# Kernel optimization log

Measured on AMD Instinct MI355X. Metric: run time of the kernel, lower is better.

The kernel has to match this reference:

```python
import jax, jax.numpy as jnp
import numpy as np

B, L, D = 2, 2048, 1024
H = 16
DH = D // H
FACTOR = 0.6
U = max(1, min(L, int(FACTOR * L)))  # 1228 selected queries


def setup_inputs() -> dict:
    key = jax.random.key(0)
    ks = jax.random.split(key, 9)
    s = 0.02
    return {
        "x": jax.random.normal(ks[0], (B, L, D), dtype=jnp.float32),
        "Wq": jax.random.normal(ks[1], (D, D), dtype=jnp.float32) * s,
        "bq": jnp.zeros((D,), dtype=jnp.float32),
        "Wk": jax.random.normal(ks[2], (D, D), dtype=jnp.float32) * s,
        "bk": jnp.zeros((D,), dtype=jnp.float32),
        "Wv": jax.random.normal(ks[3], (D, D), dtype=jnp.float32) * s,
        "bv": jnp.zeros((D,), dtype=jnp.float32),
        "Wo": jax.random.normal(ks[4], (D, D), dtype=jnp.float32) * s,
        "bo": jnp.zeros((D,), dtype=jnp.float32),
    }


def _split_heads(x):
    b, l, d = x.shape
    return x.reshape(b, l, H, DH).transpose(0, 2, 1, 3)  # [b,h,l,dh]


def reference(x, Wq, bq, Wk, bk, Wv, bv, Wo, bo):
    b, l, _ = x.shape
    scale = 1.0 / jnp.sqrt(jnp.asarray(DH, dtype=x.dtype))

    q = _split_heads(x @ Wq + bq)  # [b,h,l,dh]
    k = _split_heads(x @ Wk + bk)
    v = _split_heads(x @ Wv + bv)

    # full scores for sparsity heuristic
    scores = jnp.einsum("bhqd,bhkd->bhqk", q, k) * scale  # [b,h,l,l]
    sparsity = scores.max(axis=-1) - scores.mean(axis=-1)  # [b,h,l]

    _, top_idx = jax.lax.top_k(sparsity, U)  # [b,h,U]

    # gather selected queries, attend only on those rows
    q_sel = jnp.take_along_axis(q, top_idx[..., None], axis=2)  # [b,h,U,dh]
    scores_sel = jnp.einsum("bhud,bhkd->bhuk", q_sel, k) * scale  # [b,h,U,l]
    attn = jax.nn.softmax(scores_sel, axis=-1)
    out_sel = jnp.einsum("bhuk,bhkd->bhud", attn, v)  # [b,h,U,dh]

    # scatter back into zero-initialized output
    bi = jnp.arange(b)[:, None, None]
    hi = jnp.arange(H)[None, :, None]
    out = jnp.zeros_like(q).at[bi, hi, top_idx].set(out_sel)  # [b,h,l,dh]

    out = out.transpose(0, 2, 1, 3).reshape(b, l, D)
    return out @ Wo + bo
```

## Files before the change

kernel.cpp:

```cpp
#include <hip/hip_runtime.h>
#include <math.h>
#include <stdint.h>

#define Bn 2
#define Ln 2048
#define Dn 1024
#define Hn 16
#define DHn 64
#define Un 1228
#define BHn (Bn*Hn)
#define SCALE 0.125f
#define SXf 16.0f
#define SWf 256.0f
#define SQf 16.0f
#define SVf 16.0f
#define SPf 16.0f
#define ESC_PROJ (1.0f / 4096.0f)
#define ESC_OUT  (1.0f / 65536.0f)
#define PSC (SCALE / 256.0f)
#define QPS 88

typedef _Float16 f16;
typedef __attribute__((ext_vector_type(8))) _Float16 f16x8;
typedef __attribute__((ext_vector_type(4))) float f32x4;
struct h4s { f16 x, y, z, w; };

__device__ __forceinline__ void splitf16(float f, f16& hi, f16& lo) {
  hi = (f16)f;
  lo = (f16)(f - (float)hi);
}

__device__ __forceinline__ void gl_lds16(const void* g, void* l) {
  __builtin_amdgcn_global_load_lds(
      (const __attribute__((address_space(1))) void*)g,
      (__attribute__((address_space(3))) void*)l, 16, 0, 0);
}

#define MFMA(a, b, c) __builtin_amdgcn_mfma_f32_16x16x32_f16((a), (b), (c), 0, 0, 0)

__global__ __launch_bounds__(256) void split_kernel(
    const float* __restrict__ in, f16* __restrict__ oh, f16* __restrict__ ol, int n4) {
  int i = blockIdx.x * 256 + threadIdx.x;
  if (i >= n4) return;
  float4 v = ((const float4*)in)[i];
  h4s h, l;
  splitf16(v.x * SXf, h.x, l.x); splitf16(v.y * SXf, h.y, l.y);
  splitf16(v.z * SXf, h.z, l.z); splitf16(v.w * SXf, h.w, l.w);
  ((h4s*)oh)[i] = h; ((h4s*)ol)[i] = l;
}

__global__ __launch_bounds__(256) void tsplit_w4(
    const float* __restrict__ W0, const float* __restrict__ W1,
    const float* __restrict__ W2, const float* __restrict__ W3,
    f16* __restrict__ oh, f16* __restrict__ ol) {
  __shared__ float ts[64][65];
  const int t = threadIdx.x;
  const int r0 = blockIdx.x * 64, c0 = blockIdx.y * 64;
  const int z = blockIdx.z;
  const float* in = (z == 0) ? W0 : (z == 1) ? W1 : (z == 2) ? W2 : W3;
#pragma unroll
  for (int c = 0; c < 4; ++c) {
    int f = (c * 256 + t) * 4; int row = f >> 6, col = f & 63;
    float4 v = *(const float4*)&in[(size_t)(r0 + row) * Dn + c0 + col];
    ts[row][col] = v.x; ts[row][col + 1] = v.y; ts[row][col + 2] = v.z; ts[row][col + 3] = v.w;
  }
  __syncthreads();
#pragma unroll
  for (int c = 0; c < 4; ++c) {
    int f = (c * 256 + t) * 4; int crow = f >> 6, rcol = f & 63;
    h4s h, l;
    splitf16(ts[rcol + 0][crow] * SWf, h.x, l.x);
    splitf16(ts[rcol + 1][crow] * SWf, h.y, l.y);
    splitf16(ts[rcol + 2][crow] * SWf, h.z, l.z);
    splitf16(ts[rcol + 3][crow] * SWf, h.w, l.w);
    size_t o = (size_t)(z * 1024 + c0 + crow) * Dn + r0 + rcol;
    *(h4s*)&oh[o] = h; *(h4s*)&ol[o] = l;
  }
}

__global__ void gemm_qkv(
    const f16* __restrict__ Ah, const f16* __restrict__ Al,
    const f16* __restrict__ Bth, const f16* __restrict__ Btl,
    const float* __restrict__ bq, const float* __restrict__ bk, const float* __restrict__ bv,
    float* __restrict__ Qf, f16* __restrict__ Qbh, f16* __restrict__ Qbl,
    float* __restrict__ Kf, f16* __restrict__ Kbh, f16* __restrict__ Kbl,
    f16* __restrict__ Vh16, int K) {
  __shared__ f16 sAh[128 * 32], sAl[128 * 32], sBh[128 * 32], sBl[128 * 32];
  const int t = threadIdx.x;
  const int w = t >> 6, lane = t & 63, lm = lane & 15, q = lane >> 4;
  const int wr = w >> 1, wc = w & 1;
  const int n0 = blockIdx.x * 128, m0 = blockIdx.y * 128;
  f32x4 acc[4][4] = {};
  for (int k0 = 0; k0 < K; k0 += 32) {
    const f16* s0 = Ah + (size_t)m0 * K + k0;
    const f16* s1 = Al + (size_t)m0 * K + k0;
    const f16* s2 = Bth + (size_t)n0 * K + k0;
    const f16* s3 = Btl + (size_t)n0 * K + k0;
#pragma unroll
    for (int c = 0; c < 2; ++c) {
      int f = (c * 256 + t) * 8; int row = f >> 5, col = f & 31;
      size_t go = (size_t)row * K + col;
      gl_lds16(s0 + go, &sAh[f]);
      gl_lds16(s1 + go, &sAl[f]);
      gl_lds16(s2 + go, &sBh[f]);
      gl_lds16(s3 + go, &sBl[f]);
    }
    __syncthreads();
    f16x8 a_h[4], a_l[4], b_h[4], b_l[4];
#pragma unroll
    for (int mi = 0; mi < 4; ++mi) {
      int r = (wr * 64 + mi * 16 + lm) * 32 + q * 8;
      a_h[mi] = *(const f16x8*)&sAh[r];
      a_l[mi] = *(const f16x8*)&sAl[r];
    }
#pragma unroll
    for (int ni = 0; ni < 4; ++ni) {
      int r = (wc * 64 + ni * 16 + lm) * 32 + q * 8;
      b_h[ni] = *(const f16x8*)&sBh[r];
      b_l[ni] = *(const f16x8*)&sBl[r];
    }
#pragma unroll
    for (int mi = 0; mi < 4; ++mi)
#pragma unroll
      for (int ni = 0; ni < 4; ++ni) {
        acc[mi][ni] = MFMA(a_h[mi], b_h[ni], acc[mi][ni]);
        acc[mi][ni] = MFMA(a_h[mi], b_l[ni], acc[mi][ni]);
        acc[mi][ni] = MFMA(a_l[mi], b_h[ni], acc[mi][ni]);
      }
    __syncthreads();
  }
#pragma unroll
  for (int mi = 0; mi < 4; ++mi)
#pragma unroll
    for (int ni = 0; ni < 4; ++ni) {
      int nglob = n0 + wc * 64 + ni * 16;
      int seg = nglob >> 10;
      int c = (nglob & 1023) + lm;
      const float* bp = (seg == 0) ? bq : (seg == 1) ? bk : bv;
      float bvv = bp[c];
#pragma unroll
      for (int r = 0; r < 4; ++r) {
        int grow = m0 + wr * 64 + mi * 16 + q * 4 + r;
        float v = acc[mi][ni][r] * ESC_PROJ + bvv;
        size_t o = (size_t)grow * 1024 + c;
        if (seg == 0) {
          Qf[o] = v;
          f16 hh, ll; splitf16(v * SQf, hh, ll); Qbh[o] = hh; Qbl[o] = ll;
        } else if (seg == 1) {
          Kf[o] = v;
          f16 hh, ll; splitf16(v * SQf, hh, ll); Kbh[o] = hh; Kbl[o] = ll;
        } else {
          Vh16[o] = (f16)(v * SVf);
        }
      }
    }
}

__global__ __launch_bounds__(256) void tsplit_v(
    const f16* __restrict__ Vh16, f16* __restrict__ out) {
  __shared__ f16 ts[64][72];
  const int t = threadIdx.x;
  const int l0 = blockIdx.x * 64;
  const int bh = blockIdx.y, b = bh >> 4, h = bh & 15;
#pragma unroll
  for (int c = 0; c < 2; ++c) {
    int e = c * 256 + t; int row = e >> 3, cg = e & 7;
    *(uint4*)&ts[row][cg * 8] =
        *(const uint4*)&Vh16[((size_t)b * Ln + l0 + row) * Dn + h * DHn + cg * 8];
  }
  __syncthreads();
#pragma unroll
  for (int c = 0; c < 2; ++c) {
    int e = c * 256 + t; int drow = e >> 3, lg = e & 7;
    f16 tmp[8];
#pragma unroll
    for (int j = 0; j < 8; ++j) tmp[j] = ts[lg * 8 + j][drow];
    *(uint4*)&out[((size_t)bh * DHn + drow) * Ln + l0 + lg * 8] = *(uint4*)tmp;
  }
}

__global__ __launch_bounds__(256, 4) void gemm_a1(
    const f16* __restrict__ A,
    const f16* __restrict__ Bth, const f16* __restrict__ Btl,
    const float* __restrict__ bias, float escale,
    float* __restrict__ Cf, int M, int N, int K) {
  __shared__ f16 sA[128 * 32], sBh[64 * 32], sBl[64 * 32];
  const int t = threadIdx.x;
  const int w = t >> 6, lane = t & 63, lm = lane & 15, q = lane >> 4;
  const int wr = w >> 1, wc = w & 1;
  const int n0 = blockIdx.x * 64, m0 = blockIdx.y * 128;
  f32x4 acc[4][2] = {};
  for (int k0 = 0; k0 < K; k0 += 32) {
    const f16* s0 = A + (size_t)m0 * K + k0;
    const f16* s2 = Bth + (size_t)n0 * K + k0;
    const f16* s3 = Btl + (size_t)n0 * K + k0;
#pragma unroll
    for (int c = 0; c < 2; ++c) {
      int f = (c * 256 + t) * 8; int row = f >> 5, col = f & 31;
      gl_lds16(s0 + (size_t)row * K + col, &sA[f]);
    }
    {
      int f = t * 8; int row = f >> 5, col = f & 31;
      gl_lds16(s2 + (size_t)row * K + col, &sBh[f]);
      gl_lds16(s3 + (size_t)row * K + col, &sBl[f]);
    }
    __syncthreads();
    f16x8 a_[4], b_h[2], b_l[2];
#pragma unroll
    for (int mi = 0; mi < 4; ++mi)
      a_[mi] = *(const f16x8*)&sA[(wr * 64 + mi * 16 + lm) * 32 + q * 8];
#pragma unroll
    for (int ni = 0; ni < 2; ++ni) {
      int r = (wc * 32 + ni * 16 + lm) * 32 + q * 8;
      b_h[ni] = *(const f16x8*)&sBh[r];
      b_l[ni] = *(const f16x8*)&sBl[r];
    }
#pragma unroll
    for (int mi = 0; mi < 4; ++mi)
#pragma unroll
      for (int ni = 0; ni < 2; ++ni) {
        acc[mi][ni] = MFMA(a_[mi], b_h[ni], acc[mi][ni]);
        acc[mi][ni] = MFMA(a_[mi], b_l[ni], acc[mi][ni]);
      }
    __syncthreads();
  }
#pragma unroll
  for (int mi = 0; mi < 4; ++mi)
#pragma unroll
    for (int ni = 0; ni < 2; ++ni) {
      int gcol = n0 + wc * 32 + ni * 16 + lm;
      float bvv = bias[gcol];
#pragma unroll
      for (int r = 0; r < 4; ++r) {
        int grow = m0 + wr * 64 + mi * 16 + q * 4 + r;
        Cf[(size_t)grow * N + gcol] = acc[mi][ni][r] * escale + bvv;
      }
    }
}

__global__ __launch_bounds__(256) void ksum_part(
    const f16* __restrict__ Kh, const f16* __restrict__ Kl, float* __restrict__ ksum) {
  __shared__ float red[4][64];
  const int t = threadIdx.x, d = t & 63, seg = t >> 6;
  const int bx = blockIdx.x, bh = blockIdx.y, b = bh >> 4, h = bh & 15;
  float s = 0.f;
  const int lbase = bx * 256 + seg * 64;
  for (int r = 0; r < 64; ++r) {
    size_t o = ((size_t)b * Ln + lbase + r) * Dn + h * DHn + d;
    s += (float)Kh[o] + (float)Kl[o];
  }
  red[seg][d] = s;
  __syncthreads();
  if (t < 64) atomicAdd(&ksum[bh * DHn + t], red[0][t] + red[1][t] + red[2][t] + red[3][t]);
}

__global__ __launch_bounds__(256, 2) void attn_stats_mfma(
    const f16* __restrict__ Qh, const f16* __restrict__ Ql,
    const f16* __restrict__ Kh, const f16* __restrict__ Kl,
    const float* __restrict__ ksum,
    float* __restrict__ row_max, float* __restrict__ spars) {
  __shared__ f16 sQh[128 * 64], sQl[128 * 64], sKh[128 * 64], sKl[128 * 64];
  __shared__ float redm[128][5];
  const int t = threadIdx.x;
  const int w = t >> 6, lane = t & 63, lm = lane & 15, q = lane >> 4;
  const int bh = blockIdx.y, b = bh >> 4, h = bh & 15;
  const int q0 = blockIdx.x * 128;
  const f16* qsh = Qh + ((size_t)b * Ln + q0) * Dn + h * DHn;
  const f16* qsl = Ql + ((size_t)b * Ln + q0) * Dn + h * DHn;
#pragma unroll
  for (int c = 0; c < 4; ++c) {
    int f = (c * 256 + t) * 8; int row = f >> 6, c16 = (f >> 3) & 7;
    size_t go = (size_t)row * Dn + ((c16 ^ (row & 7)) << 3);
    gl_lds16(qsh + go, &sQh[f]);
    gl_lds16(qsl + go, &sQl[f]);
  }
  __syncthreads();
  f16x8 a_h[8][2], a_l[8][2];
#pragma unroll
  for (int mi = 0; mi < 8; ++mi)
#pragma unroll
    for (int ks = 0; ks < 2; ++ks) {
      int row = mi * 16 + lm;
      int r = row * 64 + (((ks * 4 + q) ^ (row & 7)) << 3);
      a_h[mi][ks] = *(const f16x8*)&sQh[r];
      a_l[mi][ks] = *(const f16x8*)&sQl[r];
    }
  float rmax[8][4];
#pragma unroll
  for (int mi = 0; mi < 8; ++mi)
#pragma unroll
    for (int r = 0; r < 4; ++r) rmax[mi][r] = -1e30f;

  for (int kt = 0; kt < Ln / 128; ++kt) {
    __syncthreads();
    const f16* ksh = Kh + ((size_t)b * Ln + kt * 128) * Dn + h * DHn;
    const f16* ksl = Kl + ((size_t)b * Ln + kt * 128) * Dn + h * DHn;
#pragma unroll
    for (int c = 0; c < 4; ++c) {
      int f = (c * 256 + t) * 8; int row = f >> 6, c16 = (f >> 3) & 7;
      size_t go = (size_t)row * Dn + ((c16 ^ (row & 7)) << 3);
      gl_lds16(ksh + go, &sKh[f]);
      gl_lds16(ksl + go, &sKl[f]);
    }
    __syncthreads();
#pragma unroll
    for (int ni = 0; ni < 2; ++ni) {
      int bcol = (w * 2 + ni) * 16;
      f16x8 b_h[2], b_l[2];
#pragma unroll
      for (int ks = 0; ks < 2; ++ks) {
        int row = bcol + lm;
        int r = row * 64 + (((ks * 4 + q) ^ (row & 7)) << 3);
        b_h[ks] = *(const f16x8*)&sKh[r];
        b_l[ks] = *(const f16x8*)&sKl[r];
      }
#pragma unroll
      for (int mi = 0; mi < 8; ++mi) {
        f32x4 acc = {0.f, 0.f, 0.f, 0.f};
        __builtin_amdgcn_s_setprio(1);
#pragma unroll
        for (int ks = 0; ks < 2; ++ks) {
          acc = MFMA(a_h[mi][ks], b_h[ks], acc);
          acc = MFMA(a_h[mi][ks], b_l[ks], acc);
          acc = MFMA(a_l[mi][ks], b_h[ks], acc);
        }
        __builtin_amdgcn_s_setprio(0);
#pragma unroll
        for (int r = 0; r < 4; ++r) rmax[mi][r] = fmaxf(rmax[mi][r], acc[r]);
      }
    }
  }
#pragma unroll
  for (int mi = 0; mi < 8; ++mi)
#pragma unroll
    for (int r = 0; r < 4; ++r) {
      float v = rmax[mi][r];
      v = fmaxf(v, __shfl_xor(v, 1)); v = fmaxf(v, __shfl_xor(v, 2));
      v = fmaxf(v, __shfl_xor(v, 4)); v = fmaxf(v, __shfl_xor(v, 8));
      if (lm == 0) redm[mi * 16 + q * 4 + r][w] = v;
    }
  __syncthreads();
  if (t < 128) {
    float m = fmaxf(fmaxf(redm[t][0], redm[t][1]), fmaxf(redm[t][2], redm[t][3]));
    float dot = 0.f;
    const float* kp = ksum + bh * DHn;
#pragma unroll
    for (int d = 0; d < 64; ++d) {
      int idx = t * 64 + ((((d >> 3) ^ (t & 7)) << 3) | (d & 7));
      dot += ((float)sQh[idx] + (float)sQl[idx]) * kp[d];
    }
    row_max[(size_t)bh * Ln + q0 + t] = m * PSC;
    spars[(size_t)bh * Ln + q0 + t] = m * PSC - dot * (PSC / (float)Ln);
  }
}

__global__ __launch_bounds__(1024) void topk_sort(
    const float* __restrict__ spars, int* __restrict__ top_idx, int* __restrict__ wrow) {
  __shared__ unsigned long long keys[Ln];
  const int t = threadIdx.x;
  const int bh = blockIdx.x;
  for (int i = t; i < Ln; i += 1024) {
    unsigned u = __float_as_uint(spars[(size_t)bh * Ln + i]);
    u = (u & 0x80000000u) ? ~u : (u | 0x80000000u);
    u = ~u;
    keys[i] = ((unsigned long long)u << 32) | (unsigned)i;
  }
  __syncthreads();
  for (int k = 2; k <= Ln; k <<= 1) {
    for (int j = k >> 1; j > 0; j >>= 1) {
      int i = ((t & ~(j - 1)) << 1) | (t & (j - 1));
      int ixj = i | j;
      unsigned long long a = keys[i], bb = keys[ixj];
      bool up = ((i & k) == 0);
      if ((a > bb) == up) { keys[i] = bb; keys[ixj] = a; }
      __syncthreads();
    }
  }
  for (int u = t; u < Un - 8; u += 1024)
    top_idx[(size_t)bh * Un + u] = (int)(keys[u] & 0xFFFFFFFFu);
  if (t < 16) wrow[bh * 16 + t] = (int)(keys[Un - 8 + t] & 0xFFFFFFFFu);
}

__global__ __launch_bounds__(256) void refine_rows(
    const float* __restrict__ Qf, const float* __restrict__ Kf,
    const int* __restrict__ wrow, float* __restrict__ spx) {
  __shared__ float qs[64];
  __shared__ float redm[4], reds[4];
  const int t = threadIdx.x;
  const int j = blockIdx.x, bh = blockIdx.y, b = bh >> 4, h = bh & 15;
  const int qi = wrow[bh * 16 + j];
  if (t < 64) qs[t] = Qf[((size_t)b * Ln + qi) * Dn + h * DHn + t];
  __syncthreads();
  float mx = -1e30f, sm = 0.f;
  for (int ki = t; ki < Ln; ki += 256) {
    const float* kp = &Kf[((size_t)b * Ln + ki) * Dn + h * DHn];
    float s = 0.f;
#pragma unroll
    for (int d0 = 0; d0 < 64; d0 += 4) {
      float4 k4 = *(const float4*)&kp[d0];
      s = fmaf(k4.x, qs[d0], s);
      s = fmaf(k4.y, qs[d0 + 1], s);
      s = fmaf(k4.z, qs[d0 + 2], s);
      s = fmaf(k4.w, qs[d0 + 3], s);
    }
    mx = fmaxf(mx, s); sm += s;
  }
  const int w = t >> 6, lane = t & 63;
#pragma unroll
  for (int off = 1; off < 64; off <<= 1) {
    mx = fmaxf(mx, __shfl_xor(mx, off));
    sm += __shfl_xor(sm, off);
  }
  if (lane == 0) { redm[w] = mx; reds[w] = sm; }
  __syncthreads();
  if (t == 0) {
    float m = fmaxf(fmaxf(redm[0], redm[1]), fmaxf(redm[2], redm[3]));
    float s = reds[0] + reds[1] + reds[2] + reds[3];
    spx[bh * 16 + j] = SCALE * (m - s * (1.0f / (float)Ln));
  }
}

__global__ __launch_bounds__(64) void topk_final(
    const float* __restrict__ spx, const int* __restrict__ wrow,
    int* __restrict__ top_idx) {
  const int bh = blockIdx.x;
  if (threadIdx.x != 0) return;
  float v[16]; int r[16];
#pragma unroll
  for (int j = 0; j < 16; ++j) { v[j] = spx[bh * 16 + j]; r[j] = wrow[bh * 16 + j]; }
  unsigned taken = 0;
  for (int s = 0; s < 8; ++s) {
    int best = -1;
    for (int j = 0; j < 16; ++j) {
      if (taken & (1u << j)) continue;
      if (best < 0 || v[j] > v[best] || (v[j] == v[best] && r[j] < r[best])) best = j;
    }
    taken |= 1u << best;
    top_idx[(size_t)bh * Un + (Un - 8) + s] = r[best];
  }
}

__global__ __launch_bounds__(256, 4) void attn_sel_part(
    const f16* __restrict__ Qh, const f16* __restrict__ Kh,
    const f16* __restrict__ Vth,
    const int* __restrict__ topi, const float* __restrict__ row_max,
    float* __restrict__ pO, float* __restrict__ pD) {
  __shared__ f16 sK[64 * 64], sV[64 * 64];
  __shared__ f16 sQP[64 * QPS];
  __shared__ float rmL[64];
  __shared__ int qxL[64];
  __shared__ float dred[64][5];
  const int t = threadIdx.x;
  const int w = t >> 6, lane = t & 63, lm = lane & 15, q = lane >> 4;
  const int half = blockIdx.y & 1, bh = blockIdx.y >> 1, b = bh >> 4, h = bh & 15;
  const int u0 = blockIdx.x * 64;
  const int nrows = (Un - u0 < 64) ? (Un - u0) : 64;
  if (t < 64) {
    int qi = topi[(size_t)bh * Un + ((t < nrows) ? (u0 + t) : 0)];
    qxL[t] = qi;
    rmL[t] = row_max[(size_t)bh * Ln + qi];
  }
  __syncthreads();
#pragma unroll
  for (int c = 0; c < 2; ++c) {
    int f = (c * 256 + t) * 8; int row = f >> 6, col = f & 63;
    size_t go = ((size_t)b * Ln + qxL[row]) * Dn + h * DHn + col;
    *(uint4*)&sQP[row * QPS + col] = *(const uint4*)&Qh[go];
  }
  __syncthreads();
  f16x8 aq[4][2];
#pragma unroll
  for (int mi = 0; mi < 4; ++mi)
#pragma unroll
    for (int ks = 0; ks < 2; ++ks)
      aq[mi][ks] = *(const f16x8*)&sQP[(mi * 16 + lm) * QPS + ks * 32 + q * 8];
  f32x4 oacc[4] = {};
  float dacc[4][4] = {};

  const f16* kbase = Kh + (size_t)b * Ln * Dn + h * DHn;
  const f16* vbase = Vth + (size_t)bh * DHn * Ln;
  for (int kt = 0; kt < 16; ++kt) {
    const int l0 = half * 1024 + kt * 64;
    __syncthreads();
#pragma unroll
    for (int c = 0; c < 2; ++c) {
      int f = (c * 256 + t) * 8; int row = f >> 6, c16 = (f >> 3) & 7;
      int sc = (c16 ^ (row & 7)) << 3;
      gl_lds16(kbase + (size_t)(l0 + row) * Dn + sc, &sK[f]);
      gl_lds16(vbase + (size_t)row * Ln + l0 + sc, &sV[f]);
    }
    __syncthreads();
    f16x8 kb[2];
#pragma unroll
    for (int ks = 0; ks < 2; ++ks) {
      int row = w * 16 + lm;
      kb[ks] = *(const f16x8*)&sK[row * 64 + (((ks * 4 + q) ^ (row & 7)) << 3)];
    }
#pragma unroll
    for (int mi = 0; mi < 4; ++mi) {
      f32x4 acc = {0.f, 0.f, 0.f, 0.f};
      __builtin_amdgcn_s_setprio(1);
      acc = MFMA(aq[mi][0], kb[0], acc);
      acc = MFMA(aq[mi][1], kb[1], acc);
      __builtin_amdgcn_s_setprio(0);
#pragma unroll
      for (int r = 0; r < 4; ++r) {
        int row = mi * 16 + q * 4 + r;
        float p = __expf(acc[r] * PSC - rmL[row]);
        dacc[mi][r] += p;
        sQP[row * QPS + w * 16 + lm] = (f16)(p * SPf);
      }
    }
    __syncthreads();
    f16x8 vb[2];
#pragma unroll
    for (int ks = 0; ks < 2; ++ks) {
      int row = w * 16 + lm;
      vb[ks] = *(const f16x8*)&sV[row * 64 + (((ks * 4 + q) ^ (row & 7)) << 3)];
    }
#pragma unroll
    for (int mi = 0; mi < 4; ++mi) {
      f16x8 pf0 = *(const f16x8*)&sQP[(mi * 16 + lm) * QPS + 0 * 32 + q * 8];
      f16x8 pf1 = *(const f16x8*)&sQP[(mi * 16 + lm) * QPS + 1 * 32 + q * 8];
      __builtin_amdgcn_s_setprio(1);
      oacc[mi] = MFMA(pf0, vb[0], oacc[mi]);
      oacc[mi] = MFMA(pf1, vb[1], oacc[mi]);
      __builtin_amdgcn_s_setprio(0);
    }
  }
#pragma unroll
  for (int mi = 0; mi < 4; ++mi)
#pragma unroll
    for (int r = 0; r < 4; ++r) {
      float v = dacc[mi][r];
      v += __shfl_xor(v, 1); v += __shfl_xor(v, 2);
      v += __shfl_xor(v, 4); v += __shfl_xor(v, 8);
      if (lm == 0) dred[mi * 16 + q * 4 + r][w] = v;
    }
  __syncthreads();
  const size_t pbase = ((size_t)half * BHn + bh) * 1280 + u0;
  if (t < 64)
    pD[pbase + t] = dred[t][0] + dred[t][1] + dred[t][2] + dred[t][3];
#pragma unroll
  for (int mi = 0; mi < 4; ++mi)
#pragma unroll
    for (int r = 0; r < 4; ++r) {
      int row = mi * 16 + q * 4 + r;
      pO[(pbase + row) * 64 + w * 16 + lm] = oacc[mi][r];
    }
}

__global__ __launch_bounds__(256) void attn_combine(
    const float* __restrict__ pO, const float* __restrict__ pD,
    const int* __restrict__ topi, f16* __restrict__ AOh) {
  const int t = threadIdx.x;
  const int u0 = blockIdx.x * 64, bh = blockIdx.y, b = bh >> 4, h = bh & 15;
  const int nrows = (Un - u0 < 64) ? (Un - u0) : 64;
  const int row = t >> 2, pg = t & 3;
  if (row >= nrows) return;
  int qi = topi[(size_t)bh * Un + u0 + row];
  size_t i0 = (size_t)bh * 1280 + u0 + row;
  size_t i1 = (size_t)BHn * 1280 + i0;
  float dinv = 1.0f / (pD[i0] + pD[i1]);
  const float* p0 = &pO[i0 * 64 + pg * 16];
  const float* p1 = &pO[i1 * 64 + pg * 16];
  f16 buf[16];
#pragma unroll
  for (int c = 0; c < 4; ++c) {
    float4 a = *(const float4*)&p0[c * 4];
    float4 bb = *(const float4*)&p1[c * 4];
    buf[c * 4 + 0] = (f16)((a.x + bb.x) * dinv);
    buf[c * 4 + 1] = (f16)((a.y + bb.y) * dinv);
    buf[c * 4 + 2] = (f16)((a.z + bb.z) * dinv);
    buf[c * 4 + 3] = (f16)((a.w + bb.w) * dinv);
  }
  f16* dst = &AOh[((size_t)b * Ln + qi) * Dn + h * DHn + pg * 16];
  *(uint4*)&dst[0] = *(uint4*)&buf[0];
  *(uint4*)&dst[8] = *(uint4*)&buf[8];
}

extern "C" void kernel_launch(void* const* d_in, const int* in_sizes, int n_in,
                              void* d_out, int out_size, void* d_ws, size_t ws_size,
                              hipStream_t stream) {
  (void)in_sizes; (void)n_in; (void)out_size; (void)ws_size;
  const float* x  = (const float*)d_in[0];
  const float* Wq = (const float*)d_in[1];
  const float* bq = (const float*)d_in[2];
  const float* Wk = (const float*)d_in[3];
  const float* bk = (const float*)d_in[4];
  const float* Wv = (const float*)d_in[5];
  const float* bv = (const float*)d_in[6];
  const float* Wo = (const float*)d_in[7];
  const float* bo = (const float*)d_in[8];
  float* out = (float*)d_out;

  uint8_t* p = (uint8_t*)d_ws;
  const size_t NE = (size_t)Bn * Ln * Dn;
  f16* xh = (f16*)p;  p += NE * 2;
  f16* xl = (f16*)p;  p += NE * 2;
  f16* Wt_h = (f16*)p; p += (size_t)4096 * Dn * 2;
  f16* Wt_l = (f16*)p; p += (size_t)4096 * Dn * 2;
  f16* Qbh = (f16*)p; p += NE * 2;
  f16* Qbl = (f16*)p; p += NE * 2;
  f16* Kbh = (f16*)p; p += NE * 2;
  f16* Kbl = (f16*)p; p += NE * 2;
  float* Qf = (float*)p;  p += NE * 4;
  float* Kf = (float*)p;  p += NE * 4;
  f16* Vh16 = (f16*)p; p += NE * 2;
  f16* Vth  = (f16*)p; p += NE * 2;
  float* rowmax = (float*)p; p += (size_t)BHn * Ln * 4;
  float* spars  = (float*)p; p += (size_t)BHn * Ln * 4;
  float* ksum   = (float*)p; p += (size_t)BHn * DHn * 4;
  int* topi     = (int*)p;   p += (size_t)BHn * Un * 4;
  int* wrow     = (int*)p;   p += (size_t)BHn * 16 * 4;
  float* spx    = (float*)p; p += (size_t)BHn * 16 * 4;
  float* pD     = (float*)p; p += (size_t)2 * BHn * 1280 * 4;
  float* pO = Qf;
  f16* AOh = xh;

  dim3 blk(256);
  hipLaunchKernelGGL(split_kernel, dim3((int)(NE / 4 / 256)), blk, 0, stream, x, xh, xl, (int)(NE / 4));
  hipLaunchKernelGGL(tsplit_w4, dim3(16, 16, 4), blk, 0, stream, Wq, Wk, Wv, Wo, Wt_h, Wt_l);
  hipLaunchKernelGGL(gemm_qkv, dim3(24, 32), blk, 0, stream, xh, xl, Wt_h, Wt_l,
                     bq, bk, bv, Qf, Qbh, Qbl, Kf, Kbh, Kbl, Vh16, Dn);
  hipLaunchKernelGGL(tsplit_v, dim3(Ln / 64, BHn), blk, 0, stream, Vh16, Vth);
  hipMemsetAsync(ksum, 0, (size_t)BHn * DHn * 4, stream);
  hipLaunchKernelGGL(ksum_part, dim3(8, BHn), blk, 0, stream, Kbh, Kbl, ksum);
  hipLaunchKernelGGL(attn_stats_mfma, dim3(Ln / 128, BHn), blk, 0, stream,
                     Qbh, Qbl, Kbh, Kbl, ksum, rowmax, spars);
  hipLaunchKernelGGL(topk_sort, dim3(BHn), dim3(1024), 0, stream, spars, topi, wrow);
  hipLaunchKernelGGL(refine_rows, dim3(16, BHn), blk, 0, stream, Qf, Kf, wrow, spx);
  hipLaunchKernelGGL(topk_final, dim3(BHn), dim3(64), 0, stream, spx, wrow, topi);
  hipMemsetAsync(AOh, 0, NE * 2, stream);
  hipLaunchKernelGGL(attn_sel_part, dim3((Un + 63) / 64, 2 * BHn), blk, 0, stream,
                     Qbh, Kbh, Vth, topi, rowmax, pO, pD);
  hipLaunchKernelGGL(attn_combine, dim3((Un + 63) / 64, BHn), blk, 0, stream,
                     pO, pD, topi, AOh);
  hipLaunchKernelGGL(gemm_a1, dim3(16, 32), blk, 0, stream, AOh,
                     Wt_h + (size_t)3072 * Dn, Wt_l + (size_t)3072 * Dn, bo,
                     ESC_OUT, out, Bn * Ln, Dn, Dn);
}
```

Before: 393.9 us.

## Rewrite QKV projection GEMM with double-buffered LDS pipeline and XCD-aware block remap

Replaces the simple single-buffered split-f16 QKV GEMM with a software-pipelined kernel. It uses a 64-wide K step, double-buffered LDS with XOR swizzle, and async global-to-LDS loads issued in phases interleaved with MFMA. It also uses explicit barriers and waitcnts, setprio around the MFMA bursts, and a block index remap across XCDs. The three split terms are flattened into a 48-stage sequence over K. The goal is to hide global memory latency and LDS bank conflicts in the projection GEMM, at the cost of hand-scheduled code that is harder to maintain and fragile if the dimensions change.

```diff
diff --git a/kernel.cpp b/kernel.cpp
--- a/kernel.cpp
+++ b/kernel.cpp
@@ -78,57 +78,110 @@
   }
 }
 
-__global__ void gemm_qkv(
+#define QKV_STAGE(T, u) do { \
+    const int term_ = (T) >> 4; \
+    const int chunk_ = (u) >> 1, half_ = (u) & 1; \
+    const f16* s_; \
+    if (chunk_ < 2) s_ = ((term_ == 1) ? Btl : Bth) + (size_t)(n0 + chunk_ * 64) * Dn; \
+    else            s_ = ((term_ == 2) ? Al : Ah) + (size_t)(m0 + (chunk_ - 2) * 64) * Dn; \
+    s_ += (size_t)((T) & 15) * 64 + (size_t)(half_ * 32) * Dn + goff; \
+    gl_lds16(s_, &lds[((((T) & 1) << 2) + chunk_) * 4096 + half_ * 2048 + ldst]); \
+  } while (0)
+
+#define QKV_RDA(BB, MH) do { \
+    _Pragma("unroll") for (int m2_ = 0; m2_ < 2; ++m2_) { \
+      int lr_ = ((MH) * 2 + m2_) * 16 + lm; \
+      const f16* p_ = &lds[(BB) + (2 + wr) * 4096 + lr_ * 64]; \
+      a_[m2_][0] = *(const f16x8*)(p_ + kx0); \
+      a_[m2_][1] = *(const f16x8*)(p_ + kx1); \
+    } } while (0)
+
+#define QKV_RDB(BB, NH) do { \
+    _Pragma("unroll") for (int n2_ = 0; n2_ < 2; ++n2_) { \
+      int lr_ = ((NH) * 2 + n2_) * 16 + lm; \
+      const f16* p_ = &lds[(BB) + wc * 4096 + lr_ * 64]; \
+      b_[NH][n2_][0] = *(const f16x8*)(p_ + kx0); \
+      b_[NH][n2_][1] = *(const f16x8*)(p_ + kx1); \
+    } } while (0)
+
+#define QKV_MM(MH, NH) do { \
+    _Pragma("unroll") for (int m2_ = 0; m2_ < 2; ++m2_) \
+    _Pragma("unroll") for (int n2_ = 0; n2_ < 2; ++n2_) { \
+      f32x4& A_ = acc[(MH) * 2 + m2_][(NH) * 2 + n2_]; \
+      A_ = MFMA(a_[m2_][0], b_[(NH)][n2_][0], A_); \
+      A_ = MFMA(a_[m2_][1], b_[(NH)][n2_][1], A_); \
+    } } while (0)
+
+#define QKV_PHASE(BB, MH, NH, ISS, TG, U0, VM) do { \
+    if ((MH) == 0 && (NH) == 0) { QKV_RDA(BB, 0); QKV_RDB(BB, 0); } \
+    else if ((MH) == 0 && (NH) == 1) { QKV_RDB(BB, 1); } \
+    else if ((MH) == 1 && (NH) == 0) { QKV_RDA(BB, 1); } \
+    if (ISS) { QKV_STAGE(TG, U0); QKV_STAGE(TG, (U0) + 1); } \
+    asm volatile("" ::: "memory"); \
+    __builtin_amdgcn_s_barrier(); \
+    asm volatile("s_waitcnt lgkmcnt(0)" ::: "memory"); \
+    __builtin_amdgcn_sched_barrier(0); \
+    __builtin_amdgcn_s_setprio(1); \
+    QKV_MM(MH, NH); \
+    __builtin_amdgcn_s_setprio(0); \
+    if ((VM) == 1) asm volatile("s_waitcnt vmcnt(4)" ::: "memory"); \
+    if ((VM) == 2) asm volatile("s_waitcnt vmcnt(0)" ::: "memory"); \
+    asm volatile("" ::: "memory"); \
+    __builtin_amdgcn_s_barrier(); \
+  } while (0)
+
+__global__ __launch_bounds__(256, 2) void gemm_qkv8(
     const f16* __restrict__ Ah, const f16* __restrict__ Al,
     const f16* __restrict__ Bth, const f16* __restrict__ Btl,
     const float* __restrict__ bq, const float* __restrict__ bk, const float* __restrict__ bv,
     float* __restrict__ Qf, f16* __restrict__ Qbh, f16* __restrict__ Qbl,
     float* __restrict__ Kf, f16* __restrict__ Kbh, f16* __restrict__ Kbl,
-    f16* __restrict__ Vh16, int K) {
-  __shared__ f16 sAh[128 * 32], sAl[128 * 32], sBh[128 * 32], sBl[128 * 32];
+    f16* __restrict__ Vh16) {
+  __shared__ f16 lds[32768];
   const int t = threadIdx.x;
   const int w = t >> 6, lane = t & 63, lm = lane & 15, q = lane >> 4;
   const int wr = w >> 1, wc = w & 1;
-  const int n0 = blockIdx.x * 128, m0 = blockIdx.y * 128;
+  int ob = blockIdx.x;
+  int wg = (ob & 7) * 96 + (ob >> 3);
+  const int bx = wg % 24, by = wg / 24;
+  const int n0 = bx * 128, m0 = by * 128;
+  const int srow = t >> 3;
+  const size_t goff = (size_t)srow * Dn + (size_t)((((t & 7) ^ (srow & 7)) << 3));
+  const int ldst = t * 8;
+  const int kx0 = ((q ^ (lm & 7)) << 3);
+  const int kx1 = (((4 + q) ^ (lm & 7)) << 3);
+
   f32x4 acc[4][4] = {};
-  for (int k0 = 0; k0 < K; k0 += 32) {
-    const f16* s0 = Ah + (size_t)m0 * K + k0;
-    const f16* s1 = Al + (size_t)m0 * K + k0;
-    const f16* s2 = Bth + (size_t)n0 * K + k0;
-    const f16* s3 = Btl + (size_t)n0 * K + k0;
-#pragma unroll
-    for (int c = 0; c < 2; ++c) {
-      int f = (c * 256 + t) * 8; int row = f >> 5, col = f & 31;
-      size_t go = (size_t)row * K + col;
-      gl_lds16(s0 + go, &sAh[f]);
-      gl_lds16(s1 + go, &sAl[f]);
-      gl_lds16(s2 + go, &sBh[f]);
-      gl_lds16(s3 + go, &sBl[f]);
-    }
-    __syncthreads();
-    f16x8 a_h[4], a_l[4], b_h[4], b_l[4];
-#pragma unroll
-    for (int mi = 0; mi < 4; ++mi) {
-      int r = (wr * 64 + mi * 16 + lm) * 32 + q * 8;
-      a_h[mi] = *(const f16x8*)&sAh[r];
-      a_l[mi] = *(const f16x8*)&sAl[r];
-    }
-#pragma unroll
-    for (int ni = 0; ni < 4; ++ni) {
-      int r = (wc * 64 + ni * 16 + lm) * 32 + q * 8;
-      b_h[ni] = *(const f16x8*)&sBh[r];
-      b_l[ni] = *(const f16x8*)&sBl[r];
-    }
-#pragma unroll
-    for (int mi = 0; mi < 4; ++mi)
-#pragma unroll
-      for (int ni = 0; ni < 4; ++ni) {
-        acc[mi][ni] = MFMA(a_h[mi], b_h[ni], acc[mi][ni]);
-        acc[mi][ni] = MFMA(a_h[mi], b_l[ni], acc[mi][ni]);
-        acc[mi][ni] = MFMA(a_l[mi], b_h[ni], acc[mi][ni]);
-      }
-    __syncthreads();
-  }
+  f16x8 a_[2][2], b_[2][2][2];
+
+  QKV_STAGE(0, 0); QKV_STAGE(0, 1); QKV_STAGE(0, 2); QKV_STAGE(0, 3);
+  QKV_STAGE(0, 4); QKV_STAGE(0, 5); QKV_STAGE(0, 6); QKV_STAGE(0, 7);
+  QKV_STAGE(1, 0); QKV_STAGE(1, 1); QKV_STAGE(1, 2); QKV_STAGE(1, 3);
+  asm volatile("s_waitcnt vmcnt(4)" ::: "memory");
+  asm volatile("" ::: "memory");
+  __builtin_amdgcn_s_barrier();
+
+#pragma unroll 1
+  for (int i = 0; i < 23; ++i) {
+    const int T1 = 2 * i + 1, T2 = 2 * i + 2, T3 = 2 * i + 3;
+    QKV_PHASE(0,     0, 0, 1, T1, 4, 0);
+    QKV_PHASE(0,     0, 1, 1, T1, 6, 0);
+    QKV_PHASE(0,     1, 0, 1, T2, 0, 0);
+    QKV_PHASE(0,     1, 1, 1, T2, 2, 1);
+    QKV_PHASE(16384, 0, 0, 1, T2, 4, 0);
+    QKV_PHASE(16384, 0, 1, 1, T2, 6, 0);
+    QKV_PHASE(16384, 1, 0, 1, T3, 0, 0);
+    QKV_PHASE(16384, 1, 1, 1, T3, 2, 1);
+  }
+  QKV_PHASE(0,     0, 0, 1, 47, 4, 0);
+  QKV_PHASE(0,     0, 1, 1, 47, 6, 0);
+  QKV_PHASE(0,     1, 0, 0, 0, 0, 0);
+  QKV_PHASE(0,     1, 1, 0, 0, 0, 2);
+  QKV_PHASE(16384, 0, 0, 0, 0, 0, 0);
+  QKV_PHASE(16384, 0, 1, 0, 0, 0, 0);
+  QKV_PHASE(16384, 1, 0, 0, 0, 0, 0);
+  QKV_PHASE(16384, 1, 1, 0, 0, 0, 0);
+
 #pragma unroll
   for (int mi = 0; mi < 4; ++mi)
 #pragma unroll
@@ -142,15 +195,15 @@
       for (int r = 0; r < 4; ++r) {
         int grow = m0 + wr * 64 + mi * 16 + q * 4 + r;
         float v = acc[mi][ni][r] * ESC_PROJ + bvv;
-        size_t o = (size_t)grow * 1024 + c;
+        size_t o2 = (size_t)grow * 1024 + c;
         if (seg == 0) {
-          Qf[o] = v;
-          f16 hh, ll; splitf16(v * SQf, hh, ll); Qbh[o] = hh; Qbl[o] = ll;
+          Qf[o2] = v;
+          f16 hh, ll; splitf16(v * SQf, hh, ll); Qbh[o2] = hh; Qbl[o2] = ll;
         } else if (seg == 1) {
-          Kf[o] = v;
-          f16 hh, ll; splitf16(v * SQf, hh, ll); Kbh[o] = hh; Kbl[o] = ll;
+          Kf[o2] = v;
+          f16 hh, ll; splitf16(v * SQf, hh, ll); Kbh[o2] = hh; Kbl[o2] = ll;
         } else {
-          Vh16[o] = (f16)(v * SVf);
+          Vh16[o2] = (f16)(v * SVf);
         }
       }
     }
@@ -621,8 +674,8 @@
   dim3 blk(256);
   hipLaunchKernelGGL(split_kernel, dim3((int)(NE / 4 / 256)), blk, 0, stream, x, xh, xl, (int)(NE / 4));
   hipLaunchKernelGGL(tsplit_w4, dim3(16, 16, 4), blk, 0, stream, Wq, Wk, Wv, Wo, Wt_h, Wt_l);
-  hipLaunchKernelGGL(gemm_qkv, dim3(24, 32), blk, 0, stream, xh, xl, Wt_h, Wt_l,
-                     bq, bk, bv, Qf, Qbh, Qbl, Kf, Kbh, Kbl, Vh16, Dn);
+  hipLaunchKernelGGL(gemm_qkv8, dim3(768), dim3(256), 0, stream, xh, xl, Wt_h, Wt_l,
+                     bq, bk, bv, Qf, Qbh, Qbl, Kf, Kbh, Kbl, Vh16);
   hipLaunchKernelGGL(tsplit_v, dim3(Ln / 64, BHn), blk, 0, stream, Vh16, Vth);
   hipMemsetAsync(ksum, 0, (size_t)BHn * DHn * 4, stream);
   hipLaunchKernelGGL(ksum_part, dim3(8, BHn), blk, 0, stream, Kbh, Kbl, ksum);
```

Measured after the change: 409.1 us. 3.8% more time.

## Add 8-wave pipelined QKV GEMM with double-buffered LDS and interleaved MFMA phases

Applied to the files above, without the earlier changes.

Adds a new QKV projection GEMM kernel using 512 threads (8 waves) per 128x128 tile. It stages hi/lo split operands into 128KB of double-buffered dynamic LDS with XOR swizzling and direct global-to-LDS loads. Each k-tile is split into six barrier-separated phases that interleave LDS reads, prefetch of the next tiles and MFMA work, with setprio, and uses an XCD-aware block remap. The goal is to hide global memory latency and raise MFMA utilisation in the largest GEMM. It falls back to the old kernel if the large shared-memory attribute cannot be set, and the hand-tuned waitcnt/barrier schedule carries a correctness risk.

```diff
diff --git a/kernel.cpp b/kernel.cpp
--- a/kernel.cpp
+++ b/kernel.cpp
@@ -151,6 +151,147 @@
           f16 hh, ll; splitf16(v * SQf, hh, ll); Kbh[o] = hh; Kbl[o] = ll;
         } else {
           Vh16[o] = (f16)(v * SVf);
+        }
+      }
+    }
+}
+
+#define Q8_STAGE(T, u) do { \
+    const f16* s_; \
+    if ((u) < 2)      s_ = Bth + (size_t)(n0 + (u) * 64) * Dn; \
+    else if ((u) < 4) s_ = Btl + (size_t)(n0 + ((u) - 2) * 64) * Dn; \
+    else if ((u) < 6) s_ = Ah + (size_t)(m0 + ((u) - 4) * 64) * Dn; \
+    else              s_ = Al + (size_t)(m0 + ((u) - 6) * 64) * Dn; \
+    s_ += (size_t)(T) * 64 + goff; \
+    gl_lds16(s_, &lds[(((T) & 1) << 15) + (u) * 4096 + ldst]); \
+  } while (0)
+
+#define Q8_RDA(BB, ARRC, MH, DST) do { \
+    _Pragma("unroll") for (int m2_ = 0; m2_ < 2; ++m2_) { \
+      int lr_ = (MH) * 32 + m2_ * 16 + lm; \
+      const f16* p_ = &lds[(BB) + ((ARRC) + wr) * 4096 + lr_ * 64]; \
+      DST[m2_][0] = *(const f16x8*)(p_ + kx0); \
+      DST[m2_][1] = *(const f16x8*)(p_ + kx1); \
+    } } while (0)
+
+#define Q8_RDB(BB, CH, DST) do { \
+    _Pragma("unroll") for (int n2_ = 0; n2_ < 2; ++n2_) { \
+      int row_ = wc * 32 + n2_ * 16 + lm; \
+      const f16* p_ = &lds[(BB) + ((CH) + (row_ >> 6)) * 4096 + (row_ & 63) * 64]; \
+      DST[n2_][0] = *(const f16x8*)(p_ + kx0); \
+      DST[n2_][1] = *(const f16x8*)(p_ + kx1); \
+    } } while (0)
+
+#define Q8_MM(ASET, BSET, MH) do { \
+    _Pragma("unroll") for (int m2_ = 0; m2_ < 2; ++m2_) \
+    _Pragma("unroll") for (int n2_ = 0; n2_ < 2; ++n2_) { \
+      f32x4& A_ = acc[(MH) * 2 + m2_][n2_]; \
+      A_ = MFMA(ASET[m2_][0], BSET[n2_][0], A_); \
+      A_ = MFMA(ASET[m2_][1], BSET[n2_][1], A_); \
+    } } while (0)
+
+#define Q8_MID do { \
+    asm volatile("" ::: "memory"); \
+    __builtin_amdgcn_s_barrier(); \
+    asm volatile("s_waitcnt lgkmcnt(0)" ::: "memory"); \
+    __builtin_amdgcn_sched_barrier(0); \
+    __builtin_amdgcn_s_setprio(1); \
+  } while (0)
+
+#define Q8_END(VM) do { \
+    __builtin_amdgcn_s_setprio(0); \
+    if ((VM) == 1) asm volatile("s_waitcnt vmcnt(4)" ::: "memory"); \
+    if ((VM) == 2) asm volatile("s_waitcnt vmcnt(0)" ::: "memory"); \
+    asm volatile("" ::: "memory"); \
+    __builtin_amdgcn_s_barrier(); \
+  } while (0)
+
+#define Q8_TILE(T, S1, S2, VME) do { \
+    const int BB_ = ((T) & 1) << 15; \
+     \
+    Q8_RDA(BB_, 4, 0, aA); Q8_RDB(BB_, 0, b_h); \
+    if (S1) Q8_STAGE((T) + 1, 4); \
+    Q8_MID; Q8_MM(aA, b_h, 0); Q8_END(0); \
+     \
+    Q8_RDA(BB_, 4, 1, aB); \
+    if (S1) Q8_STAGE((T) + 1, 5); \
+    Q8_MID; Q8_MM(aB, b_h, 1); Q8_END(0); \
+     \
+    Q8_RDB(BB_, 2, b_l); \
+    if (S1) { Q8_STAGE((T) + 1, 6); Q8_STAGE((T) + 1, 7); } \
+    Q8_MID; Q8_MM(aB, b_l, 1); Q8_END(0); \
+     \
+    if (S2) Q8_STAGE((T) + 2, 0); \
+    Q8_MID; Q8_MM(aA, b_l, 0); Q8_END(0); \
+     \
+    Q8_RDA(BB_, 6, 0, aA); \
+    if (S2) Q8_STAGE((T) + 2, 1); \
+    Q8_MID; Q8_MM(aA, b_h, 0); Q8_END(0); \
+     \
+    Q8_RDA(BB_, 6, 1, aB); \
+    if (S2) { Q8_STAGE((T) + 2, 2); Q8_STAGE((T) + 2, 3); } \
+    Q8_MID; Q8_MM(aB, b_h, 1); Q8_END(VME); \
+  } while (0)
+
+__global__ __launch_bounds__(512, 2) void gemm_qkv8(
+    const f16* __restrict__ Ah, const f16* __restrict__ Al,
+    const f16* __restrict__ Bth, const f16* __restrict__ Btl,
+    const float* __restrict__ bq, const float* __restrict__ bk, const float* __restrict__ bv,
+    float* __restrict__ Qf, f16* __restrict__ Qbh, f16* __restrict__ Qbl,
+    float* __restrict__ Kf, f16* __restrict__ Kbh, f16* __restrict__ Kbl,
+    f16* __restrict__ Vh16) {
+  extern __shared__ f16 lds[];
+  const int t = threadIdx.x;
+  const int w = t >> 6, lane = t & 63, lm = lane & 15, q = lane >> 4;
+  const int wr = w >> 2, wc = w & 3;
+  int ob = blockIdx.x;
+  int wg = (ob & 7) * 96 + (ob >> 3);
+  const int bx = wg % 24, by = wg / 24;
+  const int n0 = bx * 128, m0 = by * 128;
+  const int srow = t >> 3;
+  const size_t goff = (size_t)srow * Dn + (size_t)((((t & 7) ^ (srow & 7)) << 3));
+  const int ldst = t * 8;
+  const int kx0 = ((q ^ (lm & 7)) << 3);
+  const int kx1 = (((4 + q) ^ (lm & 7)) << 3);
+
+  f32x4 acc[4][2] = {};
+  f16x8 aA[2][2], aB[2][2], b_h[2][2], b_l[2][2];
+
+  Q8_STAGE(0, 0); Q8_STAGE(0, 1); Q8_STAGE(0, 2); Q8_STAGE(0, 3);
+  Q8_STAGE(0, 4); Q8_STAGE(0, 5); Q8_STAGE(0, 6); Q8_STAGE(0, 7);
+  Q8_STAGE(1, 0); Q8_STAGE(1, 1); Q8_STAGE(1, 2); Q8_STAGE(1, 3);
+  asm volatile("s_waitcnt vmcnt(4)" ::: "memory");
+  asm volatile("" ::: "memory");
+  __builtin_amdgcn_s_barrier();
+
+#pragma unroll 1
+  for (int kt = 0; kt < 14; ++kt)
+    Q8_TILE(kt, 1, 1, 1);
+  Q8_TILE(14, 1, 0, 2);
+  Q8_TILE(15, 0, 0, 0);
+
+#pragma unroll
+  for (int mi = 0; mi < 4; ++mi)
+#pragma unroll
+    for (int ni = 0; ni < 2; ++ni) {
+      int nglob = n0 + wc * 32 + ni * 16;
+      int seg = nglob >> 10;
+      int c = (nglob & 1023) + lm;
+      const float* bp = (seg == 0) ? bq : (seg == 1) ? bk : bv;
+      float bvv = bp[c];
+#pragma unroll
+      for (int r = 0; r < 4; ++r) {
+        int grow = m0 + wr * 64 + mi * 16 + q * 4 + r;
+        float v = acc[mi][ni][r] * ESC_PROJ + bvv;
+        size_t o2 = (size_t)grow * 1024 + c;
+        if (seg == 0) {
+          Qf[o2] = v;
+          f16 hh, ll; splitf16(v * SQf, hh, ll); Qbh[o2] = hh; Qbl[o2] = ll;
+        } else if (seg == 1) {
+          Kf[o2] = v;
+          f16 hh, ll; splitf16(v * SQf, hh, ll); Kbh[o2] = hh; Kbl[o2] = ll;
+        } else {
+          Vh16[o2] = (f16)(v * SVf);
         }
       }
     }
@@ -618,11 +759,24 @@
   float* pO = Qf;
   f16* AOh = xh;
 
+  static int use8 = -1;
+  if (use8 < 0) {
+    hipError_t e = hipFuncSetAttribute(
+        reinterpret_cast<const void*>(gemm_qkv8),
+        hipFuncAttributeMaxDynamicSharedMemorySize, 131072);
+    use8 = (e == hipSuccess) ? 1 : 0;
+  }
+
   dim3 blk(256);
   hipLaunchKernelGGL(split_kernel, dim3((int)(NE / 4 / 256)), blk, 0, stream, x, xh, xl, (int)(NE / 4));
   hipLaunchKernelGGL(tsplit_w4, dim3(16, 16, 4), blk, 0, stream, Wq, Wk, Wv, Wo, Wt_h, Wt_l);
-  hipLaunchKernelGGL(gemm_qkv, dim3(24, 32), blk, 0, stream, xh, xl, Wt_h, Wt_l,
-                     bq, bk, bv, Qf, Qbh, Qbl, Kf, Kbh, Kbl, Vh16, Dn);
+  if (use8) {
+    hipLaunchKernelGGL(gemm_qkv8, dim3(768), dim3(512), 131072, stream, xh, xl, Wt_h, Wt_l,
+                       bq, bk, bv, Qf, Qbh, Qbl, Kf, Kbh, Kbl, Vh16);
+  } else {
+    hipLaunchKernelGGL(gemm_qkv, dim3(24, 32), blk, 0, stream, xh, xl, Wt_h, Wt_l,
+                       bq, bk, bv, Qf, Qbh, Qbl, Kf, Kbh, Kbl, Vh16, Dn);
+  }
   hipLaunchKernelGGL(tsplit_v, dim3(Ln / 64, BHn), blk, 0, stream, Vh16, Vth);
   hipMemsetAsync(ksum, 0, (size_t)BHn * DHn * 4, stream);
   hipLaunchKernelGGL(ksum_part, dim3(8, BHn), blk, 0, stream, Kbh, Kbl, ksum);
```

Measured after the change: 407.5 us. 1.03x slower.
